# Performance work log

Hardware: AMD Instinct MI355X
Metric: run time of the kernel (lower is better)

The kernel has to match this reference:

```python
import jax, jax.numpy as jnp
import numpy as np

LSTM_DIM = 512
SENT_LEN = 384  # n words -> n+2 LSTM positions (START/STOP)


def _lstm_scan(xs, Wih, Whh, b):
    """Unidirectional LSTM over xs [T, D] -> hidden states [T, H]. torch gate order i,f,g,o."""
    H = Whh.shape[1]
    gx = xs @ Wih.T + b  # [T, 4H] precompute input contribution

    def step(carry, g_x):
        h, c = carry
        g = g_x + h @ Whh.T
        i, f, gg, o = jnp.split(g, 4)
        i = jax.nn.sigmoid(i); f = jax.nn.sigmoid(f); o = jax.nn.sigmoid(o)
        c = f * c + i * jnp.tanh(gg)
        h = o * jnp.tanh(c)
        return (h, c), h

    init = (jnp.zeros((H,), xs.dtype), jnp.zeros((H,), xs.dtype))
    _, hs = jax.lax.scan(step, init, gx)
    return hs  # [T, H]


def setup_inputs() -> dict:
    key = jax.random.key(0)
    ks = jax.random.split(key, 16)
    T = SENT_LEN + 2
    H = LSTM_DIM
    s = lambda fan: 1.0 / np.sqrt(fan)
    return {
        "tag_ids": jax.random.randint(ks[0], (T,), 0, 50, dtype=jnp.int32),
        "word_ids": jax.random.randint(ks[1], (T,), 0, 10000, dtype=jnp.int32),
        "tag_emb": jax.random.normal(ks[2], (50, 128), jnp.float32) * 0.1,
        "word_emb": jax.random.normal(ks[3], (10000, 384), jnp.float32) * 0.1,
        "Wf_ih": jax.random.normal(ks[4], (4 * H, 512), jnp.float32) * s(512),
        "Wf_hh": jax.random.normal(ks[5], (4 * H, H), jnp.float32) * s(H),
        "bf": jnp.zeros((4 * H,), jnp.float32),
        "Wb_ih": jax.random.normal(ks[6], (4 * H, 512), jnp.float32) * s(512),
        "Wb_hh": jax.random.normal(ks[7], (4 * H, H), jnp.float32) * s(H),
        "bb": jnp.zeros((4 * H,), jnp.float32),
        "W1": jax.random.normal(ks[8], (2 * H, 1024), jnp.float32) * s(2 * H),
        "b1": jnp.zeros((1024,), jnp.float32),
        "W2": jax.random.normal(ks[9], (1024, 128), jnp.float32) * s(1024),
        "b2": jnp.zeros((128,), jnp.float32),
        "V1": jax.random.normal(ks[10], (2 * H, 1024), jnp.float32) * s(2 * H),
        "c1": jnp.zeros((1024,), jnp.float32),
        "V2": jax.random.normal(ks[11], (1024, 1), jnp.float32) * s(1024),
        "c2": jnp.zeros((1,), jnp.float32),
    }


def reference(tag_ids, word_ids, tag_emb, word_emb,
              Wf_ih, Wf_hh, bf, Wb_ih, Wb_hh, bb,
              W1, b1, W2, b2, V1, c1, V2, c2):
    H = LSTM_DIM
    # Embedding lookup: concat tag+word embeddings per position  [T, 512]
    x = jnp.concatenate([tag_emb[tag_ids], word_emb[word_ids]], axis=-1)
    # Bidirectional LSTM: forward states and backward states, each [T, H]
    fwd = _lstm_scan(x, Wf_ih, Wf_hh, bf)
    bwd = _lstm_scan(x[::-1], Wb_ih, Wb_hh, bb)[::-1]
    n = x.shape[0] - 2  # sentence length
    # All spans (l, r), 0 <= l < r <= n  (batched superset of recursive decode)
    L, R = np.triu_indices(n + 1, k=1)  # static index arrays, S = n(n+1)/2
    # get_span_encoding: [fwd[r]-fwd[l] ; bwd[l+1]-bwd[r+1]]  -> [S, 2H]
    enc = jnp.concatenate([fwd[R] - fwd[L], bwd[L + 1] - bwd[R + 1]], axis=-1)
    # Feedforward forward(): x = W^T x + b per layer, ReLU between layers
    label_scores = jax.nn.relu(enc @ W1 + b1) @ W2 + b2   # [S, label_vocab]
    split_scores = jax.nn.relu(enc @ V1 + c1) @ V2 + c2   # [S, 1] per-span split scalar
    # split score of candidate s inside (l,r) = split_scores[(l,s)] + split_scores[(s,r)]
    return jnp.concatenate([label_scores, split_scores], axis=-1)  # [S, label_vocab+1]
```

## Files before the change

### kernel.cpp

```cpp
#include <hip/hip_runtime.h>

#define T_LEN 386
#define NSPAN 73920

__global__ void k_embed(const int* __restrict__ tag_ids, const int* __restrict__ word_ids,
                        const float* __restrict__ tag_emb, const float* __restrict__ word_emb,
                        float* __restrict__ x) {
    int t = blockIdx.x;
    int tid = threadIdx.x;
    int tr = tag_ids[t], wr = word_ids[t];
    x[t * 512 + tid] = tag_emb[tr * 128 + tid];
    for (int j = tid; j < 384; j += 128)
        x[t * 512 + 128 + j] = word_emb[wr * 384 + j];
}

__global__ void k_gx(const float* __restrict__ x,
                     const float* __restrict__ Wf, const float* __restrict__ bf,
                     const float* __restrict__ Wb, const float* __restrict__ bb,
                     float* __restrict__ gxf, float* __restrict__ gxb) {
    __shared__ float xs[32 * 512];
    int dir = blockIdx.z;
    const float* W = dir ? Wb : Wf;
    const float* bias = dir ? bb : bf;
    float* out = dir ? gxb : gxf;
    int nbase = blockIdx.x * 64;
    int tbase = blockIdx.y * 32;
    int tid = threadIdx.x;

    for (int i = tid; i < 32 * 128; i += 256) {
        int row = i >> 7, c4 = i & 127;
        int t = tbase + row;
        float4 v = make_float4(0.f, 0.f, 0.f, 0.f);
        if (t < T_LEN) {
            int src = dir ? (T_LEN - 1 - t) : t;
            v = ((const float4*)(x + src * 512))[c4];
        }
        ((float4*)xs)[i] = v;
    }
    __syncthreads();

    int col = tid >> 2;
    int kq = tid & 3;
    int n = nbase + col;
    const float4* wrow = (const float4*)(W + (long)n * 512);
    float acc[32];
#pragma unroll
    for (int r = 0; r < 32; ++r) acc[r] = 0.f;
#pragma unroll 2
    for (int it = 0; it < 32; ++it) {
        int k4 = it * 4 + kq;
        float4 w = wrow[k4];
#pragma unroll
        for (int r = 0; r < 32; ++r) {
            float4 xv = ((const float4*)(xs + r * 512))[k4];
            acc[r] += w.x * xv.x + w.y * xv.y + w.z * xv.z + w.w * xv.w;
        }
    }
#pragma unroll
    for (int r = 0; r < 32; ++r) {
        float v = acc[r];
        v += __shfl_xor(v, 1, 4);
        v += __shfl_xor(v, 2, 4);
        acc[r] = v;
    }
    if (kq == 0) {
        float bv = bias[n];
        for (int r = 0; r < 32; ++r) {
            int t = tbase + r;
            if (t < T_LEN) out[t * 2048 + n] = acc[r] + bv;
        }
    }
}

__global__ void k_poison(float* __restrict__ st) {
    int i = blockIdx.x * 256 + threadIdx.x;
    __hip_atomic_store(st + i, 2.0f, __ATOMIC_RELAXED, __HIP_MEMORY_SCOPE_AGENT);
}

__launch_bounds__(256, 1)
__global__ void k_scan(const float* __restrict__ gxf, const float* __restrict__ gxb,
                       const float* __restrict__ Wfhh, const float* __restrict__ Wbhh,
                       float* fwd, float* bwd) {
    __shared__ float gx_sh[T_LEN * 64];
    __shared__ float h_sh[512];
    int bid = blockIdx.x;
    int dir = bid >> 5;
    int w = bid & 31;
    int tid = threadIdx.x;
    const float* gx = dir ? gxb : gxf;
    const float* Whh = dir ? Wbhh : Wfhh;
    float* st = dir ? bwd : fwd;

    for (int idx = tid; idx < T_LEN * 64; idx += 256) {
        int t = idx >> 6, j = idx & 63;
        gx_sh[idx] = gx[t * 2048 + (j >> 4) * 512 + w * 16 + (j & 15)];
    }

    int u = tid >> 4;
    int r = tid & 15;
    int g = r >> 2;
    int kq = r & 3;
    int grow = g * 512 + w * 16 + u;
    float4 wreg[32];
    const float4* wsrc = (const float4*)(Whh + (long)grow * 512);
#pragma unroll
    for (int it = 0; it < 32; ++it) wreg[it] = wsrc[it * 4 + kq];
    float c = 0.f;
    __syncthreads();

    for (int ts = 0; ts < T_LEN; ++ts) {
        if (ts == 0) {
            h_sh[tid * 2] = 0.f;
            h_sh[tid * 2 + 1] = 0.f;
        } else {
            int srow = dir ? (T_LEN - ts) : (ts - 1);
            const float* src = st + srow * 512 + tid * 2;
            float v0, v1;
            do {
                v0 = __hip_atomic_load(src, __ATOMIC_RELAXED, __HIP_MEMORY_SCOPE_AGENT);
                v1 = __hip_atomic_load(src + 1, __ATOMIC_RELAXED, __HIP_MEMORY_SCOPE_AGENT);
            } while (v0 == 2.0f || v1 == 2.0f);
            h_sh[tid * 2] = v0;
            h_sh[tid * 2 + 1] = v1;
        }
        __syncthreads();

        const float4* hv = (const float4*)h_sh;
        float a0 = 0.f, a1 = 0.f, a2 = 0.f, a3 = 0.f;
#pragma unroll
        for (int it = 0; it < 32; ++it) {
            float4 h4 = hv[it * 4 + kq];
            float4 w4 = wreg[it];
            a0 += w4.x * h4.x; a1 += w4.y * h4.y;
            a2 += w4.z * h4.z; a3 += w4.w * h4.w;
        }
        float v = (a0 + a1) + (a2 + a3);
        v += __shfl_xor(v, 1, 4);
        v += __shfl_xor(v, 2, 4);
        float gi = __shfl(v, 0, 16)  + gx_sh[ts * 64 + u];
        float gf = __shfl(v, 4, 16)  + gx_sh[ts * 64 + 16 + u];
        float gg = __shfl(v, 8, 16)  + gx_sh[ts * 64 + 32 + u];
        float go = __shfl(v, 12, 16) + gx_sh[ts * 64 + 48 + u];
        float i_ = 1.f / (1.f + expf(-gi));
        float f_ = 1.f / (1.f + expf(-gf));
        float o_ = 1.f / (1.f + expf(-go));
        c = f_ * c + i_ * tanhf(gg);
        float h = o_ * tanhf(c);
        if (r == 0) {
            int drow = dir ? (T_LEN - 1 - ts) : ts;
            __hip_atomic_store(st + drow * 512 + w * 16 + u, h, __ATOMIC_RELAXED,
                               __HIP_MEMORY_SCOPE_AGENT);
        }
        __syncthreads();
    }
}

__global__ void k_tables(const float* __restrict__ fwd, const float* __restrict__ bwd,
                         const float* __restrict__ W1, const float* __restrict__ V1,
                         float* __restrict__ A, float* __restrict__ B,
                         float* __restrict__ AV, float* __restrict__ BV) {
    __shared__ float xs[32 * 512];
    int which = blockIdx.z;
    const float* S = (which & 1) ? bwd : fwd;
    const float* W = ((which >> 1) ? V1 : W1) + (which & 1) * 512 * 1024;
    float* out = which == 0 ? A : which == 1 ? B : which == 2 ? AV : BV;
    int nbase = blockIdx.x * 64, tbase = blockIdx.y * 32;
    int tid = threadIdx.x;

    for (int i = tid; i < 32 * 128; i += 256) {
        int row = i >> 7, c4 = i & 127;
        int t = tbase + row;
        float4 v = make_float4(0.f, 0.f, 0.f, 0.f);
        if (t < T_LEN) v = ((const float4*)(S + t * 512))[c4];
        ((float4*)xs)[i] = v;
    }
    __syncthreads();

    int cg = tid & 15;
    int rg = tid >> 4;
    int n = nbase + cg * 4;
    float4 acc0 = make_float4(0.f, 0.f, 0.f, 0.f);
    float4 acc1 = make_float4(0.f, 0.f, 0.f, 0.f);
#pragma unroll 4
    for (int k = 0; k < 512; ++k) {
        float4 wv = *(const float4*)(W + (long)k * 1024 + n);
        float x0 = xs[(rg * 2) * 512 + k];
        float x1 = xs[(rg * 2 + 1) * 512 + k];
        acc0.x += x0 * wv.x; acc0.y += x0 * wv.y; acc0.z += x0 * wv.z; acc0.w += x0 * wv.w;
        acc1.x += x1 * wv.x; acc1.y += x1 * wv.y; acc1.z += x1 * wv.z; acc1.w += x1 * wv.w;
    }
    int t0 = tbase + rg * 2, t1 = t0 + 1;
    if (t0 < T_LEN) *(float4*)(out + (long)t0 * 1024 + n) = acc0;
    if (t1 < T_LEN) *(float4*)(out + (long)t1 * 1024 + n) = acc1;
}

#define TS 64
#define KC 64
__launch_bounds__(256, 2)
__global__ void k_span(const float* __restrict__ A, const float* __restrict__ B,
                       const float* __restrict__ AV, const float* __restrict__ BV,
                       const float* __restrict__ W2, const float* __restrict__ b1,
                       const float* __restrict__ b2, const float* __restrict__ V2,
                       const float* __restrict__ c1, const float* __restrict__ c2,
                       float* __restrict__ out) {
    __shared__ float hid[TS][KC + 4];
    __shared__ float w2s[KC * 128];
    __shared__ int ls[TS], rs[TS];
    int tid = threadIdx.x;
    int wg = blockIdx.x;

    if (tid < TS) {
        int s = wg * TS + tid;
        float disc = 769.0f * 769.0f - 8.0f * (float)s;
        int l = (int)floorf((769.0f - sqrtf(disc)) * 0.5f);
        if (l < 0) l = 0;
        if (l > 383) l = 383;
#define OFF(L) ((L) * 384 - ((L) * ((L) - 1)) / 2)
        while (l + 1 <= 384 && OFF(l + 1) <= s) ++l;
        while (l > 0 && OFF(l) > s) --l;
        int r = l + 1 + (s - OFF(l));
        ls[tid] = l; rs[tid] = r;
    }
    float acc[8][4];
#pragma unroll
    for (int a = 0; a < 8; ++a)
#pragma unroll
        for (int b = 0; b < 4; ++b) acc[a][b] = 0.f;
    float vacc[4] = {0.f, 0.f, 0.f, 0.f};
    int chg = tid & 31, sgm = tid >> 5;
    int kq = tid & 15, sgb = tid >> 4;
    __syncthreads();

    for (int kb = 0; kb < 1024; kb += KC) {
        if (kb) __syncthreads();
        for (int i = tid; i < KC * 128 / 4; i += 256)
            ((float4*)w2s)[i] = ((const float4*)(W2 + kb * 128))[i];
        int ko = kb + kq * 4;
        float4 bv = *(const float4*)(b1 + ko);
        float4 cv = *(const float4*)(c1 + ko);
        float4 v2 = *(const float4*)(V2 + ko);
#pragma unroll
        for (int si = 0; si < 4; ++si) {
            int sp = sgb * 4 + si;
            int l = ls[sp], r = rs[sp];
            float4 ar = *(const float4*)(A + (long)r * 1024 + ko);
            float4 al = *(const float4*)(A + (long)l * 1024 + ko);
            float4 bl = *(const float4*)(B + (long)(l + 1) * 1024 + ko);
            float4 br = *(const float4*)(B + (long)(r + 1) * 1024 + ko);
            float4 hx;
            hx.x = fmaxf(ar.x - al.x + bl.x - br.x + bv.x, 0.f);
            hx.y = fmaxf(ar.y - al.y + bl.y - br.y + bv.y, 0.f);
            hx.z = fmaxf(ar.z - al.z + bl.z - br.z + bv.z, 0.f);
            hx.w = fmaxf(ar.w - al.w + bl.w - br.w + bv.w, 0.f);
            *(float4*)&hid[sp][kq * 4] = hx;
            float4 vr = *(const float4*)(AV + (long)r * 1024 + ko);
            float4 vl = *(const float4*)(AV + (long)l * 1024 + ko);
            float4 ul = *(const float4*)(BV + (long)(l + 1) * 1024 + ko);
            float4 ur = *(const float4*)(BV + (long)(r + 1) * 1024 + ko);
            float h0 = fmaxf(vr.x - vl.x + ul.x - ur.x + cv.x, 0.f);
            float h1 = fmaxf(vr.y - vl.y + ul.y - ur.y + cv.y, 0.f);
            float h2 = fmaxf(vr.z - vl.z + ul.z - ur.z + cv.z, 0.f);
            float h3 = fmaxf(vr.w - vl.w + ul.w - ur.w + cv.w, 0.f);
            vacc[si] += h0 * v2.x + h1 * v2.y + h2 * v2.z + h3 * v2.w;
        }
        __syncthreads();
#pragma unroll 2
        for (int k = 0; k < KC; k += 4) {
            float4 h4[8];
#pragma unroll
            for (int j2 = 0; j2 < 8; ++j2)
                h4[j2] = *(const float4*)&hid[sgm * 8 + j2][k];
#pragma unroll
            for (int kk = 0; kk < 4; ++kk) {
                float4 wv = *(const float4*)&w2s[(k + kk) * 128 + chg * 4];
#pragma unroll
                for (int j2 = 0; j2 < 8; ++j2) {
                    float hx = (&h4[j2].x)[kk];
                    acc[j2][0] += hx * wv.x; acc[j2][1] += hx * wv.y;
                    acc[j2][2] += hx * wv.z; acc[j2][3] += hx * wv.w;
                }
            }
        }
    }

    float4 b2v = *(const float4*)(b2 + chg * 4);
#pragma unroll
    for (int j2 = 0; j2 < 8; ++j2) {
        int s = wg * TS + sgm * 8 + j2;
        float* o = out + (long)s * 129 + chg * 4;
        o[0] = acc[j2][0] + b2v.x; o[1] = acc[j2][1] + b2v.y;
        o[2] = acc[j2][2] + b2v.z; o[3] = acc[j2][3] + b2v.w;
    }
    float c2v = c2[0];
#pragma unroll
    for (int si = 0; si < 4; ++si) {
        float v = vacc[si];
        for (int o = 8; o; o >>= 1) v += __shfl_xor(v, o, 16);
        if (kq == 0) out[(long)(wg * TS + sgb * 4 + si) * 129 + 128] = v + c2v;
    }
}

extern "C" void kernel_launch(void* const* d_in, const int* in_sizes, int n_in,
                              void* d_out, int out_size, void* d_ws, size_t ws_size,
                              hipStream_t stream) {
    const int* tag_ids  = (const int*)d_in[0];
    const int* word_ids = (const int*)d_in[1];
    const float* tag_emb  = (const float*)d_in[2];
    const float* word_emb = (const float*)d_in[3];
    const float* Wf_ih = (const float*)d_in[4];
    const float* Wf_hh = (const float*)d_in[5];
    const float* bf    = (const float*)d_in[6];
    const float* Wb_ih = (const float*)d_in[7];
    const float* Wb_hh = (const float*)d_in[8];
    const float* bb    = (const float*)d_in[9];
    const float* W1 = (const float*)d_in[10];
    const float* b1 = (const float*)d_in[11];
    const float* W2 = (const float*)d_in[12];
    const float* b2 = (const float*)d_in[13];
    const float* V1 = (const float*)d_in[14];
    const float* c1 = (const float*)d_in[15];
    const float* V2 = (const float*)d_in[16];
    const float* c2 = (const float*)d_in[17];

    float* ws = (float*)d_ws;
    float* x   = ws + 256;
    float* gxf = x + T_LEN * 512;
    float* gxb = gxf + T_LEN * 2048;
    float* fwd = gxb + T_LEN * 2048;
    float* bwd = fwd + T_LEN * 512;
    float* A   = bwd + T_LEN * 512;
    float* B   = A + T_LEN * 1024;
    float* AV  = B + T_LEN * 1024;
    float* BV  = AV + T_LEN * 1024;

    k_poison<<<(2 * T_LEN * 512) / 256, 256, 0, stream>>>(fwd);
    k_embed<<<T_LEN, 128, 0, stream>>>(tag_ids, word_ids, tag_emb, word_emb, x);
    k_gx<<<dim3(32, 13, 2), 256, 0, stream>>>(x, Wf_ih, bf, Wb_ih, bb, gxf, gxb);
    k_scan<<<64, 256, 0, stream>>>(gxf, gxb, Wf_hh, Wb_hh, fwd, bwd);
    k_tables<<<dim3(16, 13, 4), 256, 0, stream>>>(fwd, bwd, W1, V1, A, B, AV, BV);
    k_span<<<NSPAN / 64, 256, 0, stream>>>(A, B, AV, BV, W2, b1, b2, V2, c1, c2,
                                           (float*)d_out);
}
```

Before: 1.389 ms.

## Streamline LSTM recurrence sync with double-buffered h and vectorized coherent loads

The recurrent scan kernel now double-buffers the shared h vector, which lets it drop the second barrier per timestep. A single wave polls the global state with vectorized 32-byte loads carrying sc0/sc1 cache bits and a wave-wide any-check, instead of every thread issuing two atomic loads. Each wave packs its four h outputs into one 16-byte store rather than issuing 16 scalar atomic stores. Gate math switches to fast __expf-based sigmoid and tanh, which trades some accuracy and relies on the inline-asm cache bypass being coherent across CUs.

Result: no change. 1.386 ms (-0.3%).

```diff
diff --git a/kernel.cpp b/kernel.cpp
--- a/kernel.cpp
+++ b/kernel.cpp
@@ -2,6 +2,26 @@
 
 #define T_LEN 386
 #define NSPAN 73920
+
+typedef float v4f __attribute__((ext_vector_type(4)));
+
+__device__ inline void llc_load8(const float* p, v4f& a, v4f& b) {
+    asm volatile("global_load_dwordx4 %0, %2, off sc0 sc1\n\t"
+                 "global_load_dwordx4 %1, %2, off offset:16 sc0 sc1\n\t"
+                 "s_waitcnt vmcnt(0)"
+                 : "=&v"(a), "=&v"(b) : "v"(p) : "memory");
+}
+__device__ inline void llc_store4(float* p, v4f v) {
+    asm volatile("global_store_dwordx4 %0, %1, off sc0 sc1"
+                 :: "v"(p), "v"(v) : "memory");
+}
+
+__device__ inline float fsigmoid(float x) { return 1.f / (1.f + __expf(-x)); }
+__device__ inline float ftanh(float x) {
+    x = fminf(fmaxf(x, -15.f), 15.f);
+    float e = __expf(2.f * x);
+    return (e - 1.f) / (e + 1.f);
+}
 
 __global__ void k_embed(const int* __restrict__ tag_ids, const int* __restrict__ word_ids,
                         const float* __restrict__ tag_emb, const float* __restrict__ word_emb,
@@ -82,7 +102,7 @@
                        const float* __restrict__ Wfhh, const float* __restrict__ Wbhh,
                        float* fwd, float* bwd) {
     __shared__ float gx_sh[T_LEN * 64];
-    __shared__ float h_sh[512];
+    __shared__ float h_sh[2][512];
     int bid = blockIdx.x;
     int dir = bid >> 5;
     int w = bid & 31;
@@ -106,26 +126,32 @@
 #pragma unroll
     for (int it = 0; it < 32; ++it) wreg[it] = wsrc[it * 4 + kq];
     float c = 0.f;
-    __syncthreads();
+    int wave = tid >> 6;
 
     for (int ts = 0; ts < T_LEN; ++ts) {
-        if (ts == 0) {
-            h_sh[tid * 2] = 0.f;
-            h_sh[tid * 2 + 1] = 0.f;
-        } else {
-            int srow = dir ? (T_LEN - ts) : (ts - 1);
-            const float* src = st + srow * 512 + tid * 2;
-            float v0, v1;
-            do {
-                v0 = __hip_atomic_load(src, __ATOMIC_RELAXED, __HIP_MEMORY_SCOPE_AGENT);
-                v1 = __hip_atomic_load(src + 1, __ATOMIC_RELAXED, __HIP_MEMORY_SCOPE_AGENT);
-            } while (v0 == 2.0f || v1 == 2.0f);
-            h_sh[tid * 2] = v0;
-            h_sh[tid * 2 + 1] = v1;
+        float* hbuf = h_sh[ts & 1];
+        if (tid < 64) {
+            if (ts == 0) {
+                float4 z = make_float4(0.f, 0.f, 0.f, 0.f);
+                *(float4*)(hbuf + tid * 8) = z;
+                *(float4*)(hbuf + tid * 8 + 4) = z;
+            } else {
+                int srow = dir ? (T_LEN - ts) : (ts - 1);
+                const float* src = st + srow * 512 + tid * 8;
+                v4f a, b;
+                for (;;) {
+                    llc_load8(src, a, b);
+                    bool bad = a.x == 2.f || a.y == 2.f || a.z == 2.f || a.w == 2.f ||
+                               b.x == 2.f || b.y == 2.f || b.z == 2.f || b.w == 2.f;
+                    if (!__any(bad)) break;
+                }
+                *(v4f*)(hbuf + tid * 8) = a;
+                *(v4f*)(hbuf + tid * 8 + 4) = b;
+            }
         }
         __syncthreads();
 
-        const float4* hv = (const float4*)h_sh;
+        const float4* hv = (const float4*)hbuf;
         float a0 = 0.f, a1 = 0.f, a2 = 0.f, a3 = 0.f;
 #pragma unroll
         for (int it = 0; it < 32; ++it) {
@@ -137,21 +163,25 @@
         float v = (a0 + a1) + (a2 + a3);
         v += __shfl_xor(v, 1, 4);
         v += __shfl_xor(v, 2, 4);
-        float gi = __shfl(v, 0, 16)  + gx_sh[ts * 64 + u];
-        float gf = __shfl(v, 4, 16)  + gx_sh[ts * 64 + 16 + u];
-        float gg = __shfl(v, 8, 16)  + gx_sh[ts * 64 + 32 + u];
-        float go = __shfl(v, 12, 16) + gx_sh[ts * 64 + 48 + u];
-        float i_ = 1.f / (1.f + expf(-gi));
-        float f_ = 1.f / (1.f + expf(-gf));
-        float o_ = 1.f / (1.f + expf(-go));
-        c = f_ * c + i_ * tanhf(gg);
-        float h = o_ * tanhf(c);
-        if (r == 0) {
+        float gi = __shfl(v, (u & 3) * 16 + 0, 64)  + gx_sh[ts * 64 + u];
+        float gf = __shfl(v, (u & 3) * 16 + 4, 64)  + gx_sh[ts * 64 + 16 + u];
+        float gg = __shfl(v, (u & 3) * 16 + 8, 64)  + gx_sh[ts * 64 + 32 + u];
+        float go = __shfl(v, (u & 3) * 16 + 12, 64) + gx_sh[ts * 64 + 48 + u];
+        float i_ = fsigmoid(gi);
+        float f_ = fsigmoid(gf);
+        float o_ = fsigmoid(go);
+        c = f_ * c + i_ * ftanh(gg);
+        float h = o_ * ftanh(c);
+        float h0 = __shfl(h, 0, 64);
+        float h1 = __shfl(h, 16, 64);
+        float h2 = __shfl(h, 32, 64);
+        float h3 = __shfl(h, 48, 64);
+        if ((tid & 63) == 0) {
             int drow = dir ? (T_LEN - 1 - ts) : ts;
-            __hip_atomic_store(st + drow * 512 + w * 16 + u, h, __ATOMIC_RELAXED,
-                               __HIP_MEMORY_SCOPE_AGENT);
-        }
-        __syncthreads();
+            v4f hv4;
+            hv4.x = h0; hv4.y = h1; hv4.z = h2; hv4.w = h3;
+            llc_store4(st + drow * 512 + w * 16 + wave * 4, hv4);
+        }
     }
 }
 
```
